# Kernel tuning notes

Hardware: AMD Instinct MI355X
Metric: run time of the kernel (lower is better)

Reference implementation:

```python
import jax, jax.numpy as jnp
import numpy as np

B = 64; WIN_IN = 32; WIN_OUT = 8; NODES = 128; FEAT = 16
HID = 64; LSTM_H = 32; CLASSES = 10
N = B * WIN_IN * NODES      # 262144 total nodes in batched graph
E = 8 * N                   # 2097152 edges (avg degree 8)


def setup_inputs() -> dict:
    key = jax.random.key(0)
    ks = jax.random.split(key, 16)
    p = lambda k, s: (jax.random.normal(k, s, dtype=jnp.float32) * 0.05)
    return {
        "x": jax.random.normal(ks[0], (N, FEAT), dtype=jnp.float32),
        "edge_index": jax.random.randint(ks[1], (2, E), 0, N, dtype=jnp.int32),
        "W1": p(ks[2], (FEAT, HID)),   "b1": p(ks[3], (HID,)),
        "W2": p(ks[4], (HID, FEAT)),   "b2": p(ks[5], (FEAT,)),
        "Wih": p(ks[6], (4 * LSTM_H, NODES * FEAT)),
        "Whh": p(ks[7], (4 * LSTM_H, LSTM_H)),
        "bih": p(ks[8], (4 * LSTM_H,)), "bhh": p(ks[9], (4 * LSTM_H,)),
        "Wfc1": p(ks[10], (16, LSTM_H)), "bfc1": p(ks[11], (16,)),
        "Wfc2": p(ks[12], (CLASSES, 16)), "bfc2": p(ks[13], (CLASSES,)),
    }


def _gcn_conv(x, row, col, W, b):
    # PyG GCNConv: x' = D^-1/2 (A+I) D^-1/2 (x W) + b, deg counted at target (col)
    h = x @ W
    deg = jax.ops.segment_sum(jnp.ones(row.shape[0], jnp.float32), col, num_segments=N) + 1.0
    dinv = jax.lax.rsqrt(deg)
    msg = h[row] * (dinv[row] * dinv[col])[:, None]          # [E, F]
    agg = jax.ops.segment_sum(msg, col, num_segments=N)
    agg = agg + h * (dinv * dinv)[:, None]                   # self-loop term
    return agg + b


def _lstm(seq, Wih, Whh, bih, bhh):
    # seq: [B, T, D] -> outputs [B, T, H]; torch gate order i, f, g, o
    xs = jnp.transpose(seq, (1, 0, 2))
    h0 = jnp.zeros((seq.shape[0], LSTM_H), seq.dtype)
    bias = bih + bhh

    def step(carry, xt):
        h, c = carry
        g = xt @ Wih.T + h @ Whh.T + bias
        i, f, gg, o = jnp.split(g, 4, axis=-1)
        c = jax.nn.sigmoid(f) * c + jax.nn.sigmoid(i) * jnp.tanh(gg)
        h = jax.nn.sigmoid(o) * jnp.tanh(c)
        return (h, c), h

    _, hs = jax.lax.scan(step, (h0, h0), xs)
    return jnp.transpose(hs, (1, 0, 2))


def reference(x, edge_index, W1, b1, W2, b2, Wih, Whh, bih, bhh, Wfc1, bfc1, Wfc2, bfc2):
    row, col = edge_index[0], edge_index[1]
    h = jax.nn.relu(_gcn_conv(x, row, col, W1, b1))
    h = jax.nn.relu(_gcn_conv(h, row, col, W2, b2))
    h = h.reshape(B, WIN_IN, NODES * FEAT)
    h = _lstm(h, Wih, Whh, bih, bhh)
    h = h[:, -WIN_OUT:, :]
    h = jax.nn.relu(h @ Wfc1.T + bfc1)
    h = h @ Wfc2.T + bfc2
    return h.reshape(-1, CLASSES)
```

## Files before the change

kernel.cpp:

```cpp
#include <hip/hip_runtime.h>
#include <hip/hip_fp16.h>

#define NN      262144
#define EDGES   2097152
#define FEATD   16
#define HIDD    64
#define LSTMH   32
#define BATCH   64
#define WIN     32
#define WOUT    8
#define NCLS    10
#define ROWD    2048
#define KCHUNKS 16

#define NB2     512
#define NW      512
#define CAPB    4608
#define NBLK    256
#define CHUNK   (EDGES / NBLK)

__global__ void k_hist(const int* __restrict__ ei, int* __restrict__ hist2d) {
    __shared__ int h[NB2];
    int blk = blockIdx.x, tid = threadIdx.x;
    for (int l = tid; l < NB2; l += 256) h[l] = 0;
    __syncthreads();
    int e0 = blk * CHUNK;
    for (int i = tid; i < CHUNK; i += 256)
        atomicAdd(&h[ei[EDGES + e0 + i] >> 9], 1);
    __syncthreads();
    for (int l = tid; l < NB2; l += 256) hist2d[l * NBLK + blk] = h[l];
}

__global__ void k_scan2(int* __restrict__ hist2d, int* __restrict__ bcnt) {
    __shared__ int s[NBLK];
    int b = blockIdx.x, tid = threadIdx.x;
    int v = hist2d[b * NBLK + tid];
    s[tid] = v;
    __syncthreads();
    for (int off = 1; off < NBLK; off <<= 1) {
        int t = (tid >= off) ? s[tid - off] : 0;
        __syncthreads();
        s[tid] += t;
        __syncthreads();
    }
    hist2d[b * NBLK + tid] = s[tid] - v;
    if (tid == NBLK - 1) bcnt[b] = s[tid];
}

__global__ void k_place(const int* __restrict__ ei, const int* __restrict__ hist2d,
                        int* __restrict__ bdata) {
    __shared__ int curp[NB2];
    int blk = blockIdx.x, tid = threadIdx.x;
    for (int l = tid; l < NB2; l += 256) curp[l] = hist2d[l * NBLK + blk];
    __syncthreads();
    int e0 = blk * CHUNK;
    for (int i = tid; i < CHUNK; i += 256) {
        int r = ei[e0 + i];
        int c = ei[EDGES + e0 + i];
        int b = c >> 9;
        int p = atomicAdd(&curp[b], 1);
        if (p < CAPB) bdata[(size_t)b * CAPB + p] = (r << 9) | (c & 511);
    }
}

__global__ void __launch_bounds__(512)
k_csrsort(const int* __restrict__ bcnt, const int* __restrict__ bdata,
          int* __restrict__ rows, int* __restrict__ offp, float* __restrict__ dinv) {
    __shared__ int sidx[CAPB];
    __shared__ int sorted[CAPB];
    __shared__ int hist[NW], curp[NW], ssc[NW];
    int b = blockIdx.x, tid = threadIdx.x;
    int total = bcnt[b]; if (total > CAPB) total = CAPB;
    hist[tid] = 0;
    __syncthreads();
    const int* base = bdata + (size_t)b * CAPB;
    for (int i = tid; i < total; i += 512) {
        int w = base[i];
        sidx[i] = w;
        atomicAdd(&hist[w & 511], 1);
    }
    __syncthreads();
    int v = hist[tid];
    ssc[tid] = v;
    __syncthreads();
    for (int st = 1; st < NW; st <<= 1) {
        int t = (tid >= st) ? ssc[tid - st] : 0;
        __syncthreads();
        ssc[tid] += t;
        __syncthreads();
    }
    curp[tid] = ssc[tid] - v;
    offp[b * NW + tid] = ssc[tid];
    dinv[b * NW + tid] = rsqrtf((float)v + 1.0f);
    __syncthreads();
    for (int i = tid; i < total; i += 512) {
        int w = sidx[i];
        int pos = atomicAdd(&curp[w & 511], 1);
        sorted[pos] = w >> 9;
    }
    __syncthreads();
    for (int i = tid; i < total; i += 512) rows[(size_t)b * CAPB + i] = sorted[i];
}

__global__ void k_scale(const float* __restrict__ x, const float* __restrict__ dinv,
                        __half2* __restrict__ xsH) {
    int i = blockIdx.x * blockDim.x + threadIdx.x;
    if (i >= NN * 8) return;
    float d = dinv[i >> 3];
    float2 v = ((const float2*)x)[i];
    xsH[i] = __floats2half2_rn(v.x * d, v.y * d);
}

template<int LAYER>
__global__ void __launch_bounds__(256)
k_aggcsr(const int* __restrict__ rows, const int* __restrict__ off,
         const float* __restrict__ dinv, const __half2* __restrict__ srcH,
         const float* __restrict__ b2, __half2* __restrict__ outH) {
    int i = blockIdx.x * blockDim.x + threadIdx.x;
    if (i >= NN * 8) return;
    int n = i >> 3, f2 = i & 7;
    int begin = (n & 511) ? off[n - 1] : 0;
    int end = off[n];
    const size_t base = (size_t)(n >> 9) * CAPB;
    float2 selfv = __half22float2(srcH[(size_t)n * 8 + f2]);
    float ax = selfv.x, ay = selfv.y;
    for (size_t e = base + begin; e < base + end; ++e) {
        int r = rows[e];
        float2 v = __half22float2(srcH[(size_t)r * 8 + f2]);
        ax += v.x; ay += v.y;
    }
    float d = dinv[n];
    ax *= d; ay *= d;
    if (LAYER == 2) {
        ax = fmaxf(ax + b2[f2 * 2 + 0], 0.f);
        ay = fmaxf(ay + b2[f2 * 2 + 1], 0.f);
    }
    outH[i] = __floats2half2_rn(ax, ay);
}

__global__ void k_gcnmlp(const __half2* __restrict__ in1H, __half2* __restrict__ xsH,
                         const float* __restrict__ dinv,
                         const float* __restrict__ W1, const float* __restrict__ b1,
                         const float* __restrict__ W2) {
    __shared__ float sW1[FEATD * HIDD];
    __shared__ float sW2[HIDD * FEATD];
    __shared__ float sb1[HIDD];
    for (int l = threadIdx.x; l < FEATD * HIDD; l += blockDim.x) {
        sW1[l] = W1[l];
        sW2[l] = W2[l];
    }
    if (threadIdx.x < HIDD) sb1[threadIdx.x] = b1[threadIdx.x];
    __syncthreads();
    int n = blockIdx.x * blockDim.x + threadIdx.x;
    if (n >= NN) return;
    union { float4 f4; __half2 h2[4]; } a0, a1;
    a0.f4 = ((const float4*)(in1H + (size_t)n * 8))[0];
    a1.f4 = ((const float4*)(in1H + (size_t)n * 8))[1];
    float in[FEATD];
#pragma unroll
    for (int q = 0; q < 4; q++) {
        float2 v = __half22float2(a0.h2[q]);
        in[q * 2 + 0] = v.x; in[q * 2 + 1] = v.y;
        v = __half22float2(a1.h2[q]);
        in[8 + q * 2 + 0] = v.x; in[8 + q * 2 + 1] = v.y;
    }
    float out[FEATD];
#pragma unroll
    for (int c = 0; c < FEATD; c++) out[c] = 0.f;
#pragma unroll 8
    for (int j = 0; j < HIDD; j++) {
        float h = sb1[j];
#pragma unroll
        for (int f = 0; f < FEATD; f++) h += in[f] * sW1[f * HIDD + j];
        h = fmaxf(h, 0.f);
#pragma unroll
        for (int c = 0; c < FEATD; c++) out[c] += h * sW2[j * FEATD + c];
    }
    float dn = dinv[n];
    union { float4 f4; __half2 h2[4]; } o0, o1;
#pragma unroll
    for (int q = 0; q < 4; q++) {
        o0.h2[q] = __floats2half2_rn(out[q * 2] * dn, out[q * 2 + 1] * dn);
        o1.h2[q] = __floats2half2_rn(out[8 + q * 2] * dn, out[8 + q * 2 + 1] * dn);
    }
    ((float4*)(xsH + (size_t)n * 8))[0] = o0.f4;
    ((float4*)(xsH + (size_t)n * 8))[1] = o1.f4;
}

#define KT 32
#define KSPAN (ROWD / KCHUNKS)
__global__ void __launch_bounds__(256)
k_gemmA(const __half2* __restrict__ h2H, const float* __restrict__ Wih,
        float* __restrict__ gxp) {
    __shared__ float As[32][KT + 2];
    __shared__ float Bs[KT][128 + 4];
    int tid = threadIdx.x;
    int row0 = blockIdx.x * 32;
    int k0 = blockIdx.y * KSPAN;
    int r0 = tid & 15, r1 = r0 + 16;
    int cb = (tid >> 4) * 8;
    float acc0[8], acc1[8];
#pragma unroll
    for (int j = 0; j < 8; j++) { acc0[j] = 0.f; acc1[j] = 0.f; }
    const __half* h2 = (const __half*)h2H;
    for (int kk = 0; kk < KSPAN; kk += KT) {
        if (tid < 128) {
            int rr = tid >> 2, cc = (tid & 3) * 8;
            union { float4 f4; __half2 h2v[4]; } a;
            a.f4 = *(const float4*)(h2 + (size_t)(row0 + rr) * ROWD + k0 + kk + cc);
#pragma unroll
            for (int q = 0; q < 4; q++) {
                float2 v = __half22float2(a.h2v[q]);
                As[rr][cc + q * 2 + 0] = v.x;
                As[rr][cc + q * 2 + 1] = v.y;
            }
        }
#pragma unroll
        for (int w = 0; w < 4; w++) {
            int idx = tid + w * 256;
            int rr = idx >> 3;
            int cc = (idx & 7) * 4;
            float4 v = *(const float4*)&Wih[(size_t)rr * ROWD + k0 + kk + cc];
            Bs[cc + 0][rr] = v.x;
            Bs[cc + 1][rr] = v.y;
            Bs[cc + 2][rr] = v.z;
            Bs[cc + 3][rr] = v.w;
        }
        __syncthreads();
#pragma unroll
        for (int k = 0; k < KT; k++) {
            float a0 = As[r0][k];
            float a1 = As[r1][k];
            float4 b0 = *(const float4*)&Bs[k][cb];
            float4 b1 = *(const float4*)&Bs[k][cb + 4];
            acc0[0] += a0 * b0.x; acc0[1] += a0 * b0.y;
            acc0[2] += a0 * b0.z; acc0[3] += a0 * b0.w;
            acc0[4] += a0 * b1.x; acc0[5] += a0 * b1.y;
            acc0[6] += a0 * b1.z; acc0[7] += a0 * b1.w;
            acc1[0] += a1 * b0.x; acc1[1] += a1 * b0.y;
            acc1[2] += a1 * b0.z; acc1[3] += a1 * b0.w;
            acc1[4] += a1 * b1.x; acc1[5] += a1 * b1.y;
            acc1[6] += a1 * b1.z; acc1[7] += a1 * b1.w;
        }
        __syncthreads();
    }
    float* o0 = gxp + (size_t)blockIdx.y * (ROWD * 128) + (size_t)(row0 + r0) * 128 + cb;
    float* o1 = gxp + (size_t)blockIdx.y * (ROWD * 128) + (size_t)(row0 + r1) * 128 + cb;
    ((float4*)o0)[0] = make_float4(acc0[0], acc0[1], acc0[2], acc0[3]);
    ((float4*)o0)[1] = make_float4(acc0[4], acc0[5], acc0[6], acc0[7]);
    ((float4*)o1)[0] = make_float4(acc1[0], acc1[1], acc1[2], acc1[3]);
    ((float4*)o1)[1] = make_float4(acc1[4], acc1[5], acc1[6], acc1[7]);
}

__global__ void k_pre(const float* __restrict__ gxp, float* __restrict__ sgx) {
    int i = blockIdx.x * blockDim.x + threadIdx.x;
    if (i >= ROWD * 128) return;
    float s = 0.f;
#pragma unroll
    for (int p = 0; p < KCHUNKS; p++) s += gxp[(size_t)p * ROWD * 128 + i];
    sgx[i] = s;
}

__global__ void k_lstm(const float* __restrict__ sgx, const float* __restrict__ Whh,
                       const float* __restrict__ bih, const float* __restrict__ bhh,
                       float* __restrict__ hseq) {
    __shared__ float sWhhT[LSTMH][4 * LSTMH];
    __shared__ float sgxL[WIN * 4 * LSTMH];
    __shared__ float sh[LSTMH], sc[LSTMH], sg[4 * LSTMH];
    int b = blockIdx.x, j = threadIdx.x;
    for (int l = j; l < 4 * LSTMH * LSTMH; l += 4 * LSTMH) {
        int r = l >> 5, k = l & 31;
        sWhhT[k][r] = Whh[l];
    }
    for (int l = j; l < WIN * 128; l += 128) sgxL[l] = sgx[(size_t)b * WIN * 128 + l];
    float bias = bih[j] + bhh[j];
    if (j < LSTMH) { sh[j] = 0.f; sc[j] = 0.f; }
    __syncthreads();
    for (int t = 0; t < WIN; t++) {
        float g = bias + sgxL[t * 128 + j];
#pragma unroll
        for (int k = 0; k < LSTMH; k++) g += sWhhT[k][j] * sh[k];
        sg[j] = g;
        __syncthreads();
        if (j < LSTMH) {
            float ig = sg[j], fg = sg[32 + j], gg = sg[64 + j], og = sg[96 + j];
            float c = sc[j];
            float si = 1.f / (1.f + __expf(-ig));
            float sf = 1.f / (1.f + __expf(-fg));
            float so = 1.f / (1.f + __expf(-og));
            c = sf * c + si * tanhf(gg);
            float h = so * tanhf(c);
            sc[j] = c; sh[j] = h;
            if (t >= WIN - WOUT)
                hseq[(size_t)(b * WOUT + (t - (WIN - WOUT))) * LSTMH + j] = h;
        }
        __syncthreads();
    }
}

__global__ void k_fc(const float* __restrict__ hseq, const float* __restrict__ Wfc1,
                     const float* __restrict__ bfc1, const float* __restrict__ Wfc2,
                     const float* __restrict__ bfc2, float* __restrict__ out) {
    __shared__ float sW1[16 * 32], sb1[16], sW2[10 * 16], sb2[10];
    int tid = threadIdx.x;
    for (int l = tid; l < 16 * 32; l += blockDim.x) sW1[l] = Wfc1[l];
    if (tid < 16) sb1[tid] = bfc1[tid];
    for (int l = tid; l < 160; l += blockDim.x) sW2[l] = Wfc2[l];
    if (tid < 10) sb2[tid] = bfc2[tid];
    __syncthreads();
    int r = blockIdx.x * blockDim.x + tid;
    if (r >= BATCH * WOUT) return;
    float h[32];
#pragma unroll
    for (int k = 0; k < 32; k++) h[k] = hseq[(size_t)r * 32 + k];
    float hid[16];
#pragma unroll
    for (int j = 0; j < 16; j++) {
        float v = sb1[j];
#pragma unroll
        for (int k = 0; k < 32; k++) v += sW1[j * 32 + k] * h[k];
        hid[j] = fmaxf(v, 0.f);
    }
#pragma unroll
    for (int c = 0; c < NCLS; c++) {
        float v = sb2[c];
#pragma unroll
        for (int j = 0; j < 16; j++) v += sW2[c * 16 + j] * hid[j];
        out[(size_t)r * NCLS + c] = v;
    }
}

extern "C" void kernel_launch(void* const* d_in, const int* in_sizes, int n_in,
                              void* d_out, int out_size, void* d_ws, size_t ws_size,
                              hipStream_t stream) {
    const float* x    = (const float*)d_in[0];
    const int*   ei   = (const int*)d_in[1];
    const float* W1   = (const float*)d_in[2];
    const float* b1   = (const float*)d_in[3];
    const float* W2   = (const float*)d_in[4];
    const float* b2   = (const float*)d_in[5];
    const float* Wih  = (const float*)d_in[6];
    const float* Whh  = (const float*)d_in[7];
    const float* bih  = (const float*)d_in[8];
    const float* bhh  = (const float*)d_in[9];
    const float* Wfc1 = (const float*)d_in[10];
    const float* bfc1 = (const float*)d_in[11];
    const float* Wfc2 = (const float*)d_in[12];
    const float* bfc2 = (const float*)d_in[13];
    float* out = (float*)d_out;

    float*   ws     = (float*)d_ws;
    float*   dinv   = ws;
    int*     hist2d = (int*)(dinv + NN);
    int*     bcnt   = hist2d + NB2 * NBLK;
    int*     off    = bcnt + NB2;
    int*     rows   = off + NN;
    __half2* aggH   = (__half2*)(rows + (size_t)NB2 * CAPB);
    __half2* xsH    = aggH + (size_t)NN * 8;
    int*     bdata  = (int*)(xsH + (size_t)NN * 8);
    float*   gxp    = (float*)(bdata + (size_t)NB2 * CAPB);
    float*   sgx    = gxp + (size_t)KCHUNKS * ROWD * 128;
    float*   hseq   = sgx + ROWD * 128;

    k_hist<<<NBLK, 256, 0, stream>>>(ei, hist2d);
    k_scan2<<<NB2, NBLK, 0, stream>>>(hist2d, bcnt);
    k_place<<<NBLK, 256, 0, stream>>>(ei, hist2d, bdata);
    k_csrsort<<<NB2, 512, 0, stream>>>(bcnt, bdata, rows, off, dinv);
    k_scale<<<NN * 8 / 256, 256, 0, stream>>>(x, dinv, xsH);

    k_aggcsr<1><<<NN * 8 / 256, 256, 0, stream>>>(rows, off, dinv, xsH, b2, aggH);
    k_gcnmlp<<<NN / 256, 256, 0, stream>>>(aggH, xsH, dinv, W1, b1, W2);
    k_aggcsr<2><<<NN * 8 / 256, 256, 0, stream>>>(rows, off, dinv, xsH, b2, aggH);

    dim3 gg(ROWD / 32, KCHUNKS);
    k_gemmA<<<gg, 256, 0, stream>>>(aggH, Wih, gxp);
    k_pre<<<ROWD * 128 / 256, 256, 0, stream>>>(gxp, sgx);
    k_lstm<<<BATCH, 128, 0, stream>>>(sgx, Whh, bih, bhh, hseq);
    k_fc<<<2, 256, 0, stream>>>(hseq, Wfc1, bfc1, Wfc2, bfc2, out);
}
```

Baseline: 235.3 us.

## Use MFMA fp16 for input-gate GEMM and fuse x scaling into CSR sort

Rewrites the LSTM input-projection GEMM to use 16x16x16 fp16 MFMA instructions, with Wih pre-converted to fp16 by a new small kernel and staged whole into LDS per K-span. This replaces the scalar FP32 FMA loop and its per-tile LDS transposes. It also folds the degree-normalised fp16 conversion of x into the CSR sort kernel, which removes a separate kernel launch and a reread of dinv. Wih is now rounded to fp16, which adds precision loss, and a conversion kernel runs on every call.

```diff
diff --git a/kernel.cpp b/kernel.cpp
--- a/kernel.cpp
+++ b/kernel.cpp
@@ -12,12 +12,16 @@
 #define NCLS    10
 #define ROWD    2048
 #define KCHUNKS 16
+#define KSPAN   (ROWD / KCHUNKS)
 
 #define NB2     512
 #define NW      512
 #define CAPB    4608
 #define NBLK    256
 #define CHUNK   (EDGES / NBLK)
+
+typedef __fp16 half4v __attribute__((ext_vector_type(4)));
+typedef float  float4v __attribute__((ext_vector_type(4)));
 
 __global__ void k_hist(const int* __restrict__ ei, int* __restrict__ hist2d) {
     __shared__ int h[NB2];
@@ -65,10 +69,12 @@
 
 __global__ void __launch_bounds__(512)
 k_csrsort(const int* __restrict__ bcnt, const int* __restrict__ bdata,
-          int* __restrict__ rows, int* __restrict__ offp, float* __restrict__ dinv) {
+          int* __restrict__ rows, int* __restrict__ offp, float* __restrict__ dinv,
+          const float* __restrict__ x, __half2* __restrict__ xsH) {
     __shared__ int sidx[CAPB];
     __shared__ int sorted[CAPB];
     __shared__ int hist[NW], curp[NW], ssc[NW];
+    __shared__ float sdinv[NW];
     int b = blockIdx.x, tid = threadIdx.x;
     int total = bcnt[b]; if (total > CAPB) total = CAPB;
     hist[tid] = 0;
@@ -89,26 +95,33 @@
         ssc[tid] += t;
         __syncthreads();
     }
+    float dval = rsqrtf((float)v + 1.0f);
     curp[tid] = ssc[tid] - v;
     offp[b * NW + tid] = ssc[tid];
-    dinv[b * NW + tid] = rsqrtf((float)v + 1.0f);
+    dinv[b * NW + tid] = dval;
+    sdinv[tid] = dval;
     __syncthreads();
     for (int i = tid; i < total; i += 512) {
         int w = sidx[i];
         int pos = atomicAdd(&curp[w & 511], 1);
         sorted[pos] = w >> 9;
     }
+    for (int i = tid; i < NW * 8; i += 512) {
+        int nl = i >> 3;
+        float d = sdinv[nl];
+        float2 xv = ((const float2*)x)[(size_t)(b * NW) * 8 + i];
+        xsH[(size_t)(b * NW) * 8 + i] = __floats2half2_rn(xv.x * d, xv.y * d);
+    }
     __syncthreads();
     for (int i = tid; i < total; i += 512) rows[(size_t)b * CAPB + i] = sorted[i];
 }
 
-__global__ void k_scale(const float* __restrict__ x, const float* __restrict__ dinv,
-                        __half2* __restrict__ xsH) {
+__global__ void k_wihcvt(const float* __restrict__ Wih, __half2* __restrict__ WihH) {
     int i = blockIdx.x * blockDim.x + threadIdx.x;
-    if (i >= NN * 8) return;
-    float d = dinv[i >> 3];
-    float2 v = ((const float2*)x)[i];
-    xsH[i] = __floats2half2_rn(v.x * d, v.y * d);
+    if (i >= 128 * ROWD / 4) return;
+    float4 v = ((const float4*)Wih)[i];
+    WihH[i * 2 + 0] = __floats2half2_rn(v.x, v.y);
+    WihH[i * 2 + 1] = __floats2half2_rn(v.z, v.w);
 }
 
 template<int LAYER>
@@ -187,69 +200,50 @@
     ((float4*)(xsH + (size_t)n * 8))[1] = o1.f4;
 }
 
-#define KT 32
-#define KSPAN (ROWD / KCHUNKS)
 __global__ void __launch_bounds__(256)
-k_gemmA(const __half2* __restrict__ h2H, const float* __restrict__ Wih,
+k_gemmA(const __half* __restrict__ h2, const __half* __restrict__ WihH,
         float* __restrict__ gxp) {
-    __shared__ float As[32][KT + 2];
-    __shared__ float Bs[KT][128 + 4];
+    __shared__ __half Bs[128][KSPAN + 8];
     int tid = threadIdx.x;
     int row0 = blockIdx.x * 32;
     int k0 = blockIdx.y * KSPAN;
-    int r0 = tid & 15, r1 = r0 + 16;
-    int cb = (tid >> 4) * 8;
-    float acc0[8], acc1[8];
-#pragma unroll
-    for (int j = 0; j < 8; j++) { acc0[j] = 0.f; acc1[j] = 0.f; }
-    const __half* h2 = (const __half*)h2H;
-    for (int kk = 0; kk < KSPAN; kk += KT) {
-        if (tid < 128) {
-            int rr = tid >> 2, cc = (tid & 3) * 8;
-            union { float4 f4; __half2 h2v[4]; } a;
-            a.f4 = *(const float4*)(h2 + (size_t)(row0 + rr) * ROWD + k0 + kk + cc);
-#pragma unroll
-            for (int q = 0; q < 4; q++) {
-                float2 v = __half22float2(a.h2v[q]);
-                As[rr][cc + q * 2 + 0] = v.x;
-                As[rr][cc + q * 2 + 1] = v.y;
-            }
-        }
-#pragma unroll
-        for (int w = 0; w < 4; w++) {
-            int idx = tid + w * 256;
-            int rr = idx >> 3;
-            int cc = (idx & 7) * 4;
-            float4 v = *(const float4*)&Wih[(size_t)rr * ROWD + k0 + kk + cc];
-            Bs[cc + 0][rr] = v.x;
-            Bs[cc + 1][rr] = v.y;
-            Bs[cc + 2][rr] = v.z;
-            Bs[cc + 3][rr] = v.w;
-        }
-        __syncthreads();
-#pragma unroll
-        for (int k = 0; k < KT; k++) {
-            float a0 = As[r0][k];
-            float a1 = As[r1][k];
-            float4 b0 = *(const float4*)&Bs[k][cb];
-            float4 b1 = *(const float4*)&Bs[k][cb + 4];
-            acc0[0] += a0 * b0.x; acc0[1] += a0 * b0.y;
-            acc0[2] += a0 * b0.z; acc0[3] += a0 * b0.w;
-            acc0[4] += a0 * b1.x; acc0[5] += a0 * b1.y;
-            acc0[6] += a0 * b1.z; acc0[7] += a0 * b1.w;
-            acc1[0] += a1 * b0.x; acc1[1] += a1 * b0.y;
-            acc1[2] += a1 * b0.z; acc1[3] += a1 * b0.w;
-            acc1[4] += a1 * b1.x; acc1[5] += a1 * b1.y;
-            acc1[6] += a1 * b1.z; acc1[7] += a1 * b1.w;
-        }
-        __syncthreads();
-    }
-    float* o0 = gxp + (size_t)blockIdx.y * (ROWD * 128) + (size_t)(row0 + r0) * 128 + cb;
-    float* o1 = gxp + (size_t)blockIdx.y * (ROWD * 128) + (size_t)(row0 + r1) * 128 + cb;
-    ((float4*)o0)[0] = make_float4(acc0[0], acc0[1], acc0[2], acc0[3]);
-    ((float4*)o0)[1] = make_float4(acc0[4], acc0[5], acc0[6], acc0[7]);
-    ((float4*)o1)[0] = make_float4(acc1[0], acc1[1], acc1[2], acc1[3]);
-    ((float4*)o1)[1] = make_float4(acc1[4], acc1[5], acc1[6], acc1[7]);
+    for (int idx = tid; idx < 128 * (KSPAN / 8); idx += 256) {
+        int j = idx >> 4, c8 = (idx & 15) * 8;
+        *(float4*)&Bs[j][c8] = *(const float4*)&WihH[(size_t)j * ROWD + k0 + c8];
+    }
+    __syncthreads();
+    int w = tid >> 6;
+    int l = tid & 63;
+    int rt = w & 1;
+    int ch = w >> 1;
+    int m = l & 15;
+    int kg = l >> 4;
+    float4v acc0 = {0.f, 0.f, 0.f, 0.f};
+    float4v acc1 = {0.f, 0.f, 0.f, 0.f};
+    float4v acc2 = {0.f, 0.f, 0.f, 0.f};
+    float4v acc3 = {0.f, 0.f, 0.f, 0.f};
+    const __half* aptr = h2 + (size_t)(row0 + rt * 16 + m) * ROWD + k0 + kg * 4;
+#pragma unroll
+    for (int kk = 0; kk < KSPAN; kk += 16) {
+        half4v a = *(const half4v*)(aptr + kk);
+        half4v b0 = *(const half4v*)&Bs[ch * 64 + 0 * 16 + m][kk + kg * 4];
+        half4v b1 = *(const half4v*)&Bs[ch * 64 + 1 * 16 + m][kk + kg * 4];
+        half4v b2 = *(const half4v*)&Bs[ch * 64 + 2 * 16 + m][kk + kg * 4];
+        half4v b3 = *(const half4v*)&Bs[ch * 64 + 3 * 16 + m][kk + kg * 4];
+        acc0 = __builtin_amdgcn_mfma_f32_16x16x16f16(a, b0, acc0, 0, 0, 0);
+        acc1 = __builtin_amdgcn_mfma_f32_16x16x16f16(a, b1, acc1, 0, 0, 0);
+        acc2 = __builtin_amdgcn_mfma_f32_16x16x16f16(a, b2, acc2, 0, 0, 0);
+        acc3 = __builtin_amdgcn_mfma_f32_16x16x16f16(a, b3, acc3, 0, 0, 0);
+    }
+    float* ob = gxp + (size_t)blockIdx.y * (ROWD * 128) + (size_t)(row0 + rt * 16) * 128 + ch * 64;
+#pragma unroll
+    for (int i = 0; i < 4; i++) {
+        size_t ro = (size_t)(kg * 4 + i) * 128;
+        ob[ro + 0 * 16 + m] = acc0[i];
+        ob[ro + 1 * 16 + m] = acc1[i];
+        ob[ro + 2 * 16 + m] = acc2[i];
+        ob[ro + 3 * 16 + m] = acc3[i];
+    }
 }
 
 __global__ void k_pre(const float* __restrict__ gxp, float* __restrict__ sgx) {
@@ -361,19 +355,20 @@
     float*   gxp    = (float*)(bdata + (size_t)NB2 * CAPB);
     float*   sgx    = gxp + (size_t)KCHUNKS * ROWD * 128;
     float*   hseq   = sgx + ROWD * 128;
+    __half2* WihH   = (__half2*)(hseq + BATCH * WOUT * LSTMH);
 
     k_hist<<<NBLK, 256, 0, stream>>>(ei, hist2d);
     k_scan2<<<NB2, NBLK, 0, stream>>>(hist2d, bcnt);
     k_place<<<NBLK, 256, 0, stream>>>(ei, hist2d, bdata);
-    k_csrsort<<<NB2, 512, 0, stream>>>(bcnt, bdata, rows, off, dinv);
-    k_scale<<<NN * 8 / 256, 256, 0, stream>>>(x, dinv, xsH);
+    k_csrsort<<<NB2, 512, 0, stream>>>(bcnt, bdata, rows, off, dinv, x, xsH);
+    k_wihcvt<<<128 * ROWD / 4 / 256, 256, 0, stream>>>(Wih, WihH);
 
     k_aggcsr<1><<<NN * 8 / 256, 256, 0, stream>>>(rows, off, dinv, xsH, b2, aggH);
     k_gcnmlp<<<NN / 256, 256, 0, stream>>>(aggH, xsH, dinv, W1, b1, W2);
     k_aggcsr<2><<<NN * 8 / 256, 256, 0, stream>>>(rows, off, dinv, xsH, b2, aggH);
 
     dim3 gg(ROWD / 32, KCHUNKS);
-    k_gemmA<<<gg, 256, 0, stream>>>(aggH, Wih, gxp);
+    k_gemmA<<<gg, 256, 0, stream>>>((const __half*)aggH, (const __half*)WihH, gxp);
     k_pre<<<ROWD * 128 / 256, 256, 0, stream>>>(gxp, sgx);
     k_lstm<<<BATCH, 128, 0, stream>>>(sgx, Whh, bih, bhh, hseq);
     k_fc<<<2, 256, 0, stream>>>(hseq, Wfc1, bfc1, Wfc2, bfc2, out);
```

After: 222.3 us (median of 2 runs). -5.5%, faster.
